# Kernel optimization log

Hardware: AMD Instinct MI355X
Metric: run time of the kernel (lower is better)

The kernel has to match this reference:

```python
import jax, jax.numpy as jnp
import numpy as np

V, D, S, B = 50000, 256, 128, 64

def setup_inputs() -> dict:
    key = jax.random.key(0)
    k0, k1, k2, k3, k4 = jax.random.split(key, 5)
    return {
        "questions": jax.random.randint(k0, (B, S), 0, V),
        "q_position": jax.random.uniform(k1, (B, S), dtype=jnp.float32),
        "word_emb": jax.random.normal(k2, (V, D), dtype=jnp.float32) * 0.02,
        "cmp_emb": jax.random.normal(k3, (V, D), dtype=jnp.float32) * 0.02,
        "weighted_q": jax.random.normal(k4, (S,), dtype=jnp.float32),
    }

def reference(questions, q_position, word_emb, cmp_emb, weighted_q):
    # concat_embedding (dropout is identity in eval / p=0)
    R = word_emb[questions]                              # [B,S,D] real part
    I = cmp_emb[questions] * q_position[..., None]       # [B,S,D] imag part, scaled by position
    w = weighted_q                                       # [S] (original shape (1,S,1,1) squeezed)
    # density_matrix: weighted sum over seq of per-token complex outer products.
    # torch builds real = r r^T + i i^T, imag = i r^T - r i^T per token, then
    # weighted-sums over S; fused here as weighted batched GEMMs V^T diag(w) V.
    real = jnp.einsum('bsd,s,bse->bde', R, w, R) + jnp.einsum('bsd,s,bse->bde', I, w, I)
    imag = jnp.einsum('bsd,s,bse->bde', I, w, R) - jnp.einsum('bsd,s,bse->bde', R, w, I)
    return real, imag
```

## Files before the change

### kernel.cpp

```cpp
#include <hip/hip_runtime.h>
#include <stdint.h>
#include <stddef.h>

#define DD 256
#define SS 128
#define BB 64

typedef __bf16 bf16x8 __attribute__((ext_vector_type(8)));
typedef float  f32x4  __attribute__((ext_vector_type(4)));
typedef unsigned int u32x4 __attribute__((ext_vector_type(4)));
typedef unsigned int u32x2 __attribute__((ext_vector_type(2)));

#define LSTRIDE 136
#define BUFSZ   (128 * LSTRIDE)

__device__ __forceinline__ unsigned short f2bf(float x) {
    union { float f; unsigned u; } v; v.f = x;
    unsigned r = v.u + 0x7FFFu + ((v.u >> 16) & 1u);
    return (unsigned short)(r >> 16);
}

__global__ __launch_bounds__(256, 1)
void cmp_density_kernel(const int*   __restrict__ questions,
                        const float* __restrict__ q_position,
                        const float* __restrict__ word_emb,
                        const float* __restrict__ cmp_emb,
                        const float* __restrict__ weighted_q,
                        float*       __restrict__ out)
{
    __shared__ unsigned short s16[4 * BUFSZ];
    __shared__ int   sQ[SS];
    __shared__ float sPos[SS];
    __shared__ float sW[SS];

    const int tid = threadIdx.x;
    const int bx  = blockIdx.x;
    const int b   = bx >> 2;
    const int td  = (bx >> 1) & 1;
    const int te  = bx & 1;

    if (tid < SS) {
        sQ[tid]   = questions[b * SS + tid];
        sPos[tid] = q_position[b * SS + tid];
        sW[tid]   = weighted_q[tid];
    }
    __syncthreads();

    {
        const int sg = tid & 31;
        const int cg = tid >> 5;
        const int s0 = sg * 4;
        int q[4]; float w_[4], p_[4];
        #pragma unroll
        for (int r = 0; r < 4; ++r) {
            q[r]  = sQ[s0 + r];
            w_[r] = sW[s0 + r];
            p_[r] = sPos[s0 + r];
        }
        #pragma unroll
        for (int pass = 0; pass < 4; ++pass) {
            const float* src = (pass == 0 || pass == 2) ? word_emb : cmp_emb;
            const int cb = (pass < 2) ? td * 128 : te * 128;
            unsigned short* dst = s16 + pass * BUFSZ;
            float scl[4];
            #pragma unroll
            for (int r = 0; r < 4; ++r)
                scl[r] = (pass == 0) ? w_[r]
                       : (pass == 1) ? w_[r] * p_[r]
                       : (pass == 2) ? 1.0f : p_[r];
            #pragma unroll
            for (int it = 0; it < 4; ++it) {
                const int c4 = cg + 8 * it;
                const int cl = 4 * c4;
                f32x4 v[4];
                #pragma unroll
                for (int r = 0; r < 4; ++r)
                    v[r] = *(const f32x4*)(src + (size_t)q[r] * DD + cb + cl);
                #pragma unroll
                for (int r = 0; r < 4; ++r)
                    v[r] *= scl[r];
                #pragma unroll
                for (int j = 0; j < 4; ++j) {
                    unsigned lo = (unsigned)f2bf(v[0][j]) | ((unsigned)f2bf(v[1][j]) << 16);
                    unsigned hi = (unsigned)f2bf(v[2][j]) | ((unsigned)f2bf(v[3][j]) << 16);
                    u32x2 pk; pk.x = lo; pk.y = hi;
                    *(u32x2*)&dst[(cl + j) * LSTRIDE + s0] = pk;
                }
            }
        }
    }
    __syncthreads();

    const int lane = tid & 63;
    const int wv   = tid >> 6;
    const int wr   = wv >> 1;
    const int wc   = wv & 1;
    const int m    = lane & 15;
    const int kg   = lane >> 4;

    f32x4 accR[4][4] = {};
    f32x4 accI[4][4] = {};

    const unsigned short* pRw = s16;
    const unsigned short* pIw = s16 + BUFSZ;
    const unsigned short* pR  = s16 + 2 * BUFSZ;
    const unsigned short* pI  = s16 + 3 * BUFSZ;

    u32x4 sgnmask; sgnmask.x = sgnmask.y = sgnmask.z = sgnmask.w = 0x80008000u;

    #pragma unroll
    for (int ks = 0; ks < 4; ++ks) {
        const int k0 = ks * 32 + kg * 8;
        bf16x8 aR[4], aI[4], bR[4], bI[4], aRn[4];
        #pragma unroll
        for (int t = 0; t < 4; ++t) {
            const int ra = (wr * 64 + t * 16 + m) * LSTRIDE + k0;
            const int rb = (wc * 64 + t * 16 + m) * LSTRIDE + k0;
            aR[t] = *(const bf16x8*)(pRw + ra);
            aI[t] = *(const bf16x8*)(pIw + ra);
            bR[t] = *(const bf16x8*)(pR  + rb);
            bI[t] = *(const bf16x8*)(pI  + rb);
            u32x4 raw = __builtin_bit_cast(u32x4, aR[t]);
            raw ^= sgnmask;
            aRn[t] = __builtin_bit_cast(bf16x8, raw);
        }
        #pragma unroll
        for (int di = 0; di < 4; ++di) {
            #pragma unroll
            for (int ei = 0; ei < 4; ++ei) {
                accR[di][ei] = __builtin_amdgcn_mfma_f32_16x16x32_bf16(aR[di],  bR[ei], accR[di][ei], 0, 0, 0);
                accR[di][ei] = __builtin_amdgcn_mfma_f32_16x16x32_bf16(aI[di],  bI[ei], accR[di][ei], 0, 0, 0);
                accI[di][ei] = __builtin_amdgcn_mfma_f32_16x16x32_bf16(aI[di],  bR[ei], accI[di][ei], 0, 0, 0);
                accI[di][ei] = __builtin_amdgcn_mfma_f32_16x16x32_bf16(aRn[di], bI[ei], accI[di][ei], 0, 0, 0);
            }
        }
    }

    float* outR = out + (size_t)b * DD * DD;
    float* outI = out + (size_t)BB * DD * DD + (size_t)b * DD * DD;
    const int d0 = td * 128 + wr * 64;
    const int e0 = te * 128 + wc * 64;
    #pragma unroll
    for (int di = 0; di < 4; ++di) {
        #pragma unroll
        for (int ei = 0; ei < 4; ++ei) {
            const int e = e0 + ei * 16 + m;
            #pragma unroll
            for (int r = 0; r < 4; ++r) {
                const int d = d0 + di * 16 + kg * 4 + r;
                outR[d * DD + e] = accR[di][ei][r];
                outI[d * DD + e] = accI[di][ei][r];
            }
        }
    }
}

extern "C" void kernel_launch(void* const* d_in, const int* in_sizes, int n_in,
                              void* d_out, int out_size, void* d_ws, size_t ws_size,
                              hipStream_t stream) {
    const int*   questions  = (const int*)d_in[0];
    const float* q_position = (const float*)d_in[1];
    const float* word_emb   = (const float*)d_in[2];
    const float* cmp_emb    = (const float*)d_in[3];
    const float* weighted_q = (const float*)d_in[4];
    float* out = (float*)d_out;
    (void)in_sizes; (void)n_in; (void)d_ws; (void)ws_size; (void)out_size;

    cmp_density_kernel<<<dim3(BB * 4), dim3(256), 0, stream>>>(
        questions, q_position, word_emb, cmp_emb, weighted_q, out);
}
```

Measured before the change: 136.5 us.

## Split sequence staging in halves and overlap second-half gathers with MFMA

Embedding gathers are split into two sequence halves. The first half is staged to shared memory, then the second half's global gathers are interleaved with MFMA work on the first half's K-steps. Index, position and weight loads now go straight to registers, which drops the small shared arrays and one barrier. The aim is to hide gather latency behind tensor-core work, at the cost of more live registers (two staging buffers plus 32 accumulators) and a more rigid instruction schedule.

Result: no change. 135.5 us (-0.7%).

```diff
diff --git a/kernel.cpp b/kernel.cpp
--- a/kernel.cpp
+++ b/kernel.cpp
@@ -14,10 +14,75 @@
 #define LSTRIDE 136
 #define BUFSZ   (128 * LSTRIDE)
 
-__device__ __forceinline__ unsigned short f2bf(float x) {
+__device__ __forceinline__ unsigned f2bf(float x) {
     union { float f; unsigned u; } v; v.f = x;
     unsigned r = v.u + 0x7FFFu + ((v.u >> 16) & 1u);
-    return (unsigned short)(r >> 16);
+    return r >> 16;
+}
+
+__device__ __forceinline__ void issue_loads(const float* __restrict__ src, const int4 q,
+                                            int cb, int cg, f32x4 v[2][4]) {
+    #pragma unroll
+    for (int it = 0; it < 2; ++it) {
+        const int cl = cb + 4 * (cg + 16 * it);
+        v[it][0] = *(const f32x4*)(src + (size_t)q.x * DD + cl);
+        v[it][1] = *(const f32x4*)(src + (size_t)q.y * DD + cl);
+        v[it][2] = *(const f32x4*)(src + (size_t)q.z * DD + cl);
+        v[it][3] = *(const f32x4*)(src + (size_t)q.w * DD + cl);
+    }
+}
+
+__device__ __forceinline__ void cvt_write(unsigned short* __restrict__ dst, const f32x4 scl,
+                                          int s0, int cg, f32x4 v[2][4]) {
+    #pragma unroll
+    for (int it = 0; it < 2; ++it) {
+        const int cll = 4 * (cg + 16 * it);
+        f32x4 a = v[it][0] * scl[0];
+        f32x4 b = v[it][1] * scl[1];
+        f32x4 c = v[it][2] * scl[2];
+        f32x4 d = v[it][3] * scl[3];
+        #pragma unroll
+        for (int j = 0; j < 4; ++j) {
+            u32x2 pk;
+            pk.x = f2bf(a[j]) | (f2bf(b[j]) << 16);
+            pk.y = f2bf(c[j]) | (f2bf(d[j]) << 16);
+            *(u32x2*)&dst[(cll + j) * LSTRIDE + s0] = pk;
+        }
+    }
+}
+
+template <int KS, int DI0>
+__device__ __forceinline__ void mfma_part(const unsigned short* __restrict__ s,
+                                          int wr, int wc, int m, int kg,
+                                          f32x4 accR[4][4], f32x4 accI[4][4]) {
+    const int k0 = KS * 32 + kg * 8;
+    const unsigned short* pRw = s;
+    const unsigned short* pIw = s + BUFSZ;
+    const unsigned short* pR  = s + 2 * BUFSZ;
+    const unsigned short* pI  = s + 3 * BUFSZ;
+    bf16x8 bR[4], bI[4];
+    #pragma unroll
+    for (int t = 0; t < 4; ++t) {
+        const int rb = (wc * 64 + t * 16 + m) * LSTRIDE + k0;
+        bR[t] = *(const bf16x8*)(pR + rb);
+        bI[t] = *(const bf16x8*)(pI + rb);
+    }
+    #pragma unroll
+    for (int dd = 0; dd < 2; ++dd) {
+        const int di = DI0 + dd;
+        const int ra = (wr * 64 + di * 16 + m) * LSTRIDE + k0;
+        bf16x8 aR = *(const bf16x8*)(pRw + ra);
+        bf16x8 aI = *(const bf16x8*)(pIw + ra);
+        u32x4 raw = __builtin_bit_cast(u32x4, aR) ^ 0x80008000u;
+        bf16x8 aRn = __builtin_bit_cast(bf16x8, raw);
+        #pragma unroll
+        for (int ei = 0; ei < 4; ++ei) {
+            accR[di][ei] = __builtin_amdgcn_mfma_f32_16x16x32_bf16(aR,  bR[ei], accR[di][ei], 0, 0, 0);
+            accR[di][ei] = __builtin_amdgcn_mfma_f32_16x16x32_bf16(aI,  bI[ei], accR[di][ei], 0, 0, 0);
+            accI[di][ei] = __builtin_amdgcn_mfma_f32_16x16x32_bf16(aI,  bR[ei], accI[di][ei], 0, 0, 0);
+            accI[di][ei] = __builtin_amdgcn_mfma_f32_16x16x32_bf16(aRn, bI[ei], accI[di][ei], 0, 0, 0);
+        }
+    }
 }
 
 __global__ __launch_bounds__(256, 1)
@@ -28,10 +93,7 @@
                         const float* __restrict__ weighted_q,
                         float*       __restrict__ out)
 {
-    __shared__ unsigned short s16[4 * BUFSZ];
-    __shared__ int   sQ[SS];
-    __shared__ float sPos[SS];
-    __shared__ float sW[SS];
+    __shared__ __align__(16) unsigned short s16[4 * BUFSZ];
 
     const int tid = threadIdx.x;
     const int bx  = blockIdx.x;
@@ -39,58 +101,8 @@
     const int td  = (bx >> 1) & 1;
     const int te  = bx & 1;
 
-    if (tid < SS) {
-        sQ[tid]   = questions[b * SS + tid];
-        sPos[tid] = q_position[b * SS + tid];
-        sW[tid]   = weighted_q[tid];
-    }
-    __syncthreads();
-
-    {
-        const int sg = tid & 31;
-        const int cg = tid >> 5;
-        const int s0 = sg * 4;
-        int q[4]; float w_[4], p_[4];
-        #pragma unroll
-        for (int r = 0; r < 4; ++r) {
-            q[r]  = sQ[s0 + r];
-            w_[r] = sW[s0 + r];
-            p_[r] = sPos[s0 + r];
-        }
-        #pragma unroll
-        for (int pass = 0; pass < 4; ++pass) {
-            const float* src = (pass == 0 || pass == 2) ? word_emb : cmp_emb;
-            const int cb = (pass < 2) ? td * 128 : te * 128;
-            unsigned short* dst = s16 + pass * BUFSZ;
-            float scl[4];
-            #pragma unroll
-            for (int r = 0; r < 4; ++r)
-                scl[r] = (pass == 0) ? w_[r]
-                       : (pass == 1) ? w_[r] * p_[r]
-                       : (pass == 2) ? 1.0f : p_[r];
-            #pragma unroll
-            for (int it = 0; it < 4; ++it) {
-                const int c4 = cg + 8 * it;
-                const int cl = 4 * c4;
-                f32x4 v[4];
-                #pragma unroll
-                for (int r = 0; r < 4; ++r)
-                    v[r] = *(const f32x4*)(src + (size_t)q[r] * DD + cb + cl);
-                #pragma unroll
-                for (int r = 0; r < 4; ++r)
-                    v[r] *= scl[r];
-                #pragma unroll
-                for (int j = 0; j < 4; ++j) {
-                    unsigned lo = (unsigned)f2bf(v[0][j]) | ((unsigned)f2bf(v[1][j]) << 16);
-                    unsigned hi = (unsigned)f2bf(v[2][j]) | ((unsigned)f2bf(v[3][j]) << 16);
-                    u32x2 pk; pk.x = lo; pk.y = hi;
-                    *(u32x2*)&dst[(cl + j) * LSTRIDE + s0] = pk;
-                }
-            }
-        }
-    }
-    __syncthreads();
-
+    const int sg = tid & 15;
+    const int cg = tid >> 4;
     const int lane = tid & 63;
     const int wv   = tid >> 6;
     const int wr   = wv >> 1;
@@ -98,43 +110,47 @@
     const int m    = lane & 15;
     const int kg   = lane >> 4;
 
+    const int4  q0 = *(const int4*)(questions + b * SS + 4 * sg);
+    const int4  q1 = *(const int4*)(questions + b * SS + 64 + 4 * sg);
+    const f32x4 p0 = *(const f32x4*)(q_position + b * SS + 4 * sg);
+    const f32x4 p1 = *(const f32x4*)(q_position + b * SS + 64 + 4 * sg);
+    const f32x4 w0 = *(const f32x4*)(weighted_q + 4 * sg);
+    const f32x4 w1 = *(const f32x4*)(weighted_q + 64 + 4 * sg);
+    const f32x4 ones = {1.f, 1.f, 1.f, 1.f};
+
+    f32x4 vA[2][4], vB[2][4];
+
+    issue_loads(word_emb, q0, td * 128, cg, vA);
+    issue_loads(cmp_emb,  q0, td * 128, cg, vB);
+    cvt_write(s16 + 0 * BUFSZ, w0,      4 * sg, cg, vA);
+    cvt_write(s16 + 1 * BUFSZ, w0 * p0, 4 * sg, cg, vB);
+    issue_loads(word_emb, q0, te * 128, cg, vA);
+    issue_loads(cmp_emb,  q0, te * 128, cg, vB);
+    cvt_write(s16 + 2 * BUFSZ, ones, 4 * sg, cg, vA);
+    cvt_write(s16 + 3 * BUFSZ, p0,   4 * sg, cg, vB);
+    __syncthreads();
+
     f32x4 accR[4][4] = {};
     f32x4 accI[4][4] = {};
 
-    const unsigned short* pRw = s16;
-    const unsigned short* pIw = s16 + BUFSZ;
-    const unsigned short* pR  = s16 + 2 * BUFSZ;
-    const unsigned short* pI  = s16 + 3 * BUFSZ;
+    issue_loads(word_emb, q1, td * 128, cg, vA);
+    mfma_part<0, 0>(s16, wr, wc, m, kg, accR, accI);
+    cvt_write(s16 + 0 * BUFSZ, w1, 64 + 4 * sg, cg, vA);
+    issue_loads(cmp_emb, q1, td * 128, cg, vB);
+    mfma_part<0, 2>(s16, wr, wc, m, kg, accR, accI);
+    cvt_write(s16 + 1 * BUFSZ, w1 * p1, 64 + 4 * sg, cg, vB);
+    issue_loads(word_emb, q1, te * 128, cg, vA);
+    mfma_part<1, 0>(s16, wr, wc, m, kg, accR, accI);
+    cvt_write(s16 + 2 * BUFSZ, ones, 64 + 4 * sg, cg, vA);
+    issue_loads(cmp_emb, q1, te * 128, cg, vB);
+    mfma_part<1, 2>(s16, wr, wc, m, kg, accR, accI);
+    cvt_write(s16 + 3 * BUFSZ, p1, 64 + 4 * sg, cg, vB);
+    __syncthreads();
 
-    u32x4 sgnmask; sgnmask.x = sgnmask.y = sgnmask.z = sgnmask.w = 0x80008000u;
-
-    #pragma unroll
-    for (int ks = 0; ks < 4; ++ks) {
-        const int k0 = ks * 32 + kg * 8;
-        bf16x8 aR[4], aI[4], bR[4], bI[4], aRn[4];
-        #pragma unroll
-        for (int t = 0; t < 4; ++t) {
-            const int ra = (wr * 64 + t * 16 + m) * LSTRIDE + k0;
-            const int rb = (wc * 64 + t * 16 + m) * LSTRIDE + k0;
-            aR[t] = *(const bf16x8*)(pRw + ra);
-            aI[t] = *(const bf16x8*)(pIw + ra);
-            bR[t] = *(const bf16x8*)(pR  + rb);
-            bI[t] = *(const bf16x8*)(pI  + rb);
-            u32x4 raw = __builtin_bit_cast(u32x4, aR[t]);
-            raw ^= sgnmask;
-            aRn[t] = __builtin_bit_cast(bf16x8, raw);
-        }
-        #pragma unroll
-        for (int di = 0; di < 4; ++di) {
-            #pragma unroll
-            for (int ei = 0; ei < 4; ++ei) {
-                accR[di][ei] = __builtin_amdgcn_mfma_f32_16x16x32_bf16(aR[di],  bR[ei], accR[di][ei], 0, 0, 0);
-                accR[di][ei] = __builtin_amdgcn_mfma_f32_16x16x32_bf16(aI[di],  bI[ei], accR[di][ei], 0, 0, 0);
-                accI[di][ei] = __builtin_amdgcn_mfma_f32_16x16x32_bf16(aI[di],  bR[ei], accI[di][ei], 0, 0, 0);
-                accI[di][ei] = __builtin_amdgcn_mfma_f32_16x16x32_bf16(aRn[di], bI[ei], accI[di][ei], 0, 0, 0);
-            }
-        }
-    }
+    mfma_part<2, 0>(s16, wr, wc, m, kg, accR, accI);
+    mfma_part<2, 2>(s16, wr, wc, m, kg, accR, accI);
+    mfma_part<3, 0>(s16, wr, wc, m, kg, accR, accI);
+    mfma_part<3, 2>(s16, wr, wc, m, kg, accR, accI);
 
     float* outR = out + (size_t)b * DD * DD;
     float* outI = out + (size_t)BB * DD * DD + (size_t)b * DD * DD;
```
